# Kernel tuning notes

Measured on AMD Instinct MI355X. Metric: run time of the kernel, lower is better.

The kernel has to match this reference:

```python
import jax, jax.numpy as jnp
import numpy as np

N_NODES = 50000
N_EDGES = 800000


def setup_inputs() -> dict:
    key = jax.random.key(0)
    ks = jax.random.split(key, 8)
    x = jax.random.normal(ks[0], (N_NODES, 128), dtype=jnp.float32)
    edge_index = jax.random.randint(ks[1], (2, N_EDGES), 0, N_NODES, dtype=jnp.int64)
    # Glorot-ish scaled weights (GCNConv uses glorot init)
    W1 = jax.random.normal(ks[2], (128, 128), dtype=jnp.float32) * 0.08
    W2 = jax.random.normal(ks[3], (128, 128), dtype=jnp.float32) * 0.08
    W3 = jax.random.normal(ks[4], (128, 64), dtype=jnp.float32) * 0.08
    b1 = jnp.zeros((128,), jnp.float32)
    b2 = jnp.zeros((128,), jnp.float32)
    b3 = jnp.zeros((64,), jnp.float32)
    return {"x": x, "W1": W1, "b1": b1, "W2": W2, "b2": b2,
            "W3": W3, "b3": b3, "edge_index": edge_index}


def _gcn_layer(x, W, b, src, dst, norm, n):
    # GCNConv: out = D^{-1/2} (A+I) D^{-1/2} (x W) + b
    h = x @ W                                   # [N, F_out]
    msg = h[src] * norm[:, None]                # gather + scale per edge
    agg = jax.ops.segment_sum(msg, dst, num_segments=n)  # scatter-add
    return agg + b


def reference(x, W1, b1, W2, b2, W3, b3, edge_index):
    n = x.shape[0]
    loops = jnp.arange(n, dtype=edge_index.dtype)
    src = jnp.concatenate([edge_index[0], loops])  # add self-loops (PyG default)
    dst = jnp.concatenate([edge_index[1], loops])
    # symmetric normalization from in-degree (incl. self-loops)
    deg = jax.ops.segment_sum(jnp.ones_like(dst, dtype=x.dtype), dst, num_segments=n)
    dis = jnp.where(deg > 0, jax.lax.rsqrt(deg), 0.0)
    norm = dis[src] * dis[dst]                   # [E+N]

    h = jax.nn.relu(_gcn_layer(x, W1, b1, src, dst, norm, n))
    # dropout(p=0.5) is identity in eval mode
    h = jax.nn.relu(_gcn_layer(h, W2, b2, src, dst, norm, n))
    h = _gcn_layer(h, W3, b3, src, dst, norm, n)
    return jax.nn.log_softmax(h, axis=1)
```

## Files before the change

kernel.cpp:

```cpp
#include <hip/hip_runtime.h>
#include <hip/hip_bf16.h>
#include <cstdint>

typedef unsigned int uint32;
typedef unsigned short ushort;
typedef __attribute__((ext_vector_type(8))) short short8;
typedef __attribute__((ext_vector_type(4))) float f32x4;

#define EPB 4096
#define SLACK 3840

__device__ inline ushort bf16r(float f) {
    uint32 u = __float_as_uint(f);
    u += 0x7fff + ((u >> 16) & 1);
    return (ushort)(u >> 16);
}
__device__ inline uint32 pack_bf16(float a, float b) {
    return (uint32)bf16r(a) | ((uint32)bf16r(b) << 16);
}
__device__ inline float bf_lo(uint32 w) { return __uint_as_float(w << 16); }
__device__ inline float bf_hi(uint32 w) { return __uint_as_float(w & 0xffff0000u); }


__global__ __launch_bounds__(256) void k_bhist_prep(
        const int* __restrict__ dstv, int* __restrict__ hglob, int e, int nbE,
        const float* __restrict__ W1, const float* __restrict__ W2, const float* __restrict__ W3,
        ushort* __restrict__ Wt1, ushort* __restrict__ Wt2, ushort* __restrict__ Wt3,
        ushort* __restrict__ hsb, ushort* __restrict__ hs3, int n) {
    __shared__ int h[256];
    int bid = blockIdx.x, t = threadIdx.x;
    if (bid < nbE) {
        h[t] = 0;
        __syncthreads();
        int b0 = bid * EPB;
#pragma unroll
        for (int i = 0; i < EPB / 256; ++i) {
            int idx = b0 + i * 256 + t;
            if (idx < e) atomicAdd(&h[dstv[idx] >> 8], 1);
        }
        __syncthreads();
        hglob[bid * 256 + t] = h[t];
    } else {
        int wb = bid - nbE;
        if (wb < 3) {
            const float* W = wb == 0 ? W1 : (wb == 1 ? W2 : W3);
            ushort* Wt = wb == 0 ? Wt1 : (wb == 1 ? Wt2 : Wt3);
            int F = wb == 2 ? 64 : 128;
            for (int i = t; i < 128 * F; i += 256) {
                int k = i / F, c = i % F;
                Wt[c * 128 + k] = bf16r(W[i]);
            }
        } else {
            if (t < 128) hsb[(size_t)n * 128 + t] = 0;
            if (t < 64)  hs3[(size_t)n * 64 + t] = 0;
        }
    }
}


__global__ __launch_bounds__(256) void k_bscan(const int* __restrict__ hglob, int nbE,
                                               int* __restrict__ bpre, int* __restrict__ bcur,
                                               int nb, int e) {
    __shared__ int s[256];
    int t = threadIdx.x;
    int v = 0;
    for (int b = 0; b < nbE; ++b) v += hglob[b * 256 + t];
    s[t] = v;
    __syncthreads();
    for (int off = 1; off < 256; off <<= 1) {
        int a = (t >= off) ? s[t - off] : 0;
        __syncthreads();
        s[t] += a;
        __syncthreads();
    }
    if (t < nb) { bpre[t] = s[t] - v; bcur[t] = s[t] - v; }
    if (t == 0) bpre[nb] = e;
}


__global__ __launch_bounds__(256) void k_partition(const int* __restrict__ srcv,
                                                   const int* __restrict__ dstv,
                                                   int* __restrict__ bcur,
                                                   uint2* __restrict__ pairs, int e) {
    __shared__ int h[256], base[256], cur[256];
    int t = threadIdx.x;
    h[t] = 0; cur[t] = 0;
    __syncthreads();
    int s[EPB / 256], d[EPB / 256];
    int b0 = blockIdx.x * EPB;
#pragma unroll
    for (int i = 0; i < EPB / 256; ++i) {
        int idx = b0 + i * 256 + t;
        if (idx < e) {
            s[i] = srcv[idx]; d[i] = dstv[idx];
            atomicAdd(&h[d[i] >> 8], 1);
        } else d[i] = -1;
    }
    __syncthreads();
    if (h[t]) base[t] = atomicAdd(&bcur[t], h[t]);
    __syncthreads();
#pragma unroll
    for (int i = 0; i < EPB / 256; ++i) {
        if (d[i] >= 0) {
            int b = d[i] >> 8;
            int sl = atomicAdd(&cur[b], 1);
            pairs[base[b] + sl] = make_uint2((unsigned)s[i], (unsigned)d[i]);
        }
    }
}


__global__ __launch_bounds__(256) void k_bfinish(const uint2* __restrict__ pairs,
                                                 const int* __restrict__ bpre,
                                                 int2* __restrict__ rps, float* __restrict__ dis,
                                                 int* __restrict__ col, int n) {
    __shared__ int c[256], sc[256], cur[256];
    int t = threadIdx.x;
    c[t] = 0; cur[t] = 0;
    __syncthreads();
    int wb = blockIdx.x << 8;
    int e0 = bpre[blockIdx.x], e1 = bpre[blockIdx.x + 1];
    for (int i = e0 + t; i < e1; i += 256) atomicAdd(&c[(int)pairs[i].y - wb], 1);
    __syncthreads();
    int own = c[t];
    int pad = (own + 15) & ~15;
    sc[t] = pad;
    __syncthreads();
    for (int off = 1; off < 256; off <<= 1) {
        int a = (t >= off) ? sc[t - off] : 0;
        __syncthreads();
        sc[t] += a;
        __syncthreads();
    }
    int start = bpre[blockIdx.x] + blockIdx.x * SLACK + sc[t] - pad;
    __syncthreads();
    sc[t] = start;
    int v = wb + t;
    if (v < n) {
        rps[v] = make_int2(start, start + pad);
        dis[v] = rsqrtf((float)(own + 1));
    }
    __syncthreads();
    for (int i = e0 + t; i < e1; i += 256) {
        uint2 p = pairs[i];
        int bl = (int)p.y - wb;
        int sl = atomicAdd(&cur[bl], 1);
        col[sc[bl] + sl] = (int)p.x;
    }
    __syncthreads();
    for (int i = own; i < pad; ++i) col[start + i] = n;
}


template <int FOUT, bool BF16IN>
__global__ __launch_bounds__(256) void k_gemm_mfma(
        const void* __restrict__ Xv, const ushort* __restrict__ Wt,
        const float* __restrict__ dis, ushort* __restrict__ Yb, int n) {
    constexpr int CT = FOUT / 16;
    int lane = threadIdx.x & 63;
    int wv = threadIdx.x >> 6;
    int r16 = lane & 15, kg = lane >> 4;
    int rowA = blockIdx.x * 64 + wv * 16 + r16;
    int ra = min(rowA, n - 1);
    short8 afr[4];
    if (BF16IN) {
        const ushort* Xb = (const ushort*)Xv;
#pragma unroll
        for (int ks = 0; ks < 4; ++ks)
            afr[ks] = *(const short8*)(Xb + (size_t)ra * 128 + ks * 32 + kg * 8);
    } else {
        const float* Xf = (const float*)Xv;
#pragma unroll
        for (int ks = 0; ks < 4; ++ks) {
            const float* p = Xf + (size_t)ra * 128 + ks * 32 + kg * 8;
            float4 f0 = *(const float4*)p;
            float4 f1 = *(const float4*)(p + 4);
            short8 a;
            a[0] = (short)bf16r(f0.x); a[1] = (short)bf16r(f0.y);
            a[2] = (short)bf16r(f0.z); a[3] = (short)bf16r(f0.w);
            a[4] = (short)bf16r(f1.x); a[5] = (short)bf16r(f1.y);
            a[6] = (short)bf16r(f1.z); a[7] = (short)bf16r(f1.w);
            afr[ks] = a;
        }
    }
    f32x4 acc[CT];
#pragma unroll
    for (int c = 0; c < CT; ++c) acc[c] = (f32x4){0.f, 0.f, 0.f, 0.f};
#pragma unroll
    for (int ks = 0; ks < 4; ++ks) {
#pragma unroll
        for (int c = 0; c < CT; ++c) {
            short8 b = *(const short8*)(Wt + (c * 16 + r16) * 128 + ks * 32 + kg * 8);
            acc[c] = __builtin_amdgcn_mfma_f32_16x16x32_bf16(afr[ks], b, acc[c], 0, 0, 0);
        }
    }
    int rbase = blockIdx.x * 64 + wv * 16 + kg * 4;
#pragma unroll
    for (int j = 0; j < 4; ++j) {
        int row = rbase + j;
        if (row < n) {
            float d = dis[row];
#pragma unroll
            for (int c = 0; c < CT; ++c)
                Yb[(size_t)row * FOUT + c * 16 + r16] = bf16r(acc[c][j] * d);
        }
    }
}


__global__ __launch_bounds__(256) void k_agg_relu128(
        const uint32* __restrict__ hb, const int2* __restrict__ rps,
        const int* __restrict__ col, const float* __restrict__ dis,
        const float* __restrict__ bias, uint32* __restrict__ outb, int n) {
    int wid = threadIdx.x >> 6;
    int lane = threadIdx.x & 63;
    int v = blockIdx.x * 4 + wid;
    if (v >= n) return;
    uint32 mv = hb[(size_t)v * 64 + lane];
    float ax = bf_lo(mv), ay = bf_hi(mv);
    int2 se = rps[v];
    int s = __builtin_amdgcn_readfirstlane(se.x);
    int e = __builtin_amdgcn_readfirstlane(se.y);
    for (int k = s; k < e; k += 16) {
        uint32 m[16];
#pragma unroll
        for (int j = 0; j < 16; ++j) {
            int u = col[k + j];
            m[j] = hb[(size_t)u * 64 + lane];
        }
#pragma unroll
        for (int j = 0; j < 16; ++j) { ax += bf_lo(m[j]); ay += bf_hi(m[j]); }
    }
    float d = dis[v];
    float2 b = ((const float2*)bias)[lane];
    float ox = fmaxf(d * ax + b.x, 0.f);
    float oy = fmaxf(d * ay + b.y, 0.f);
    outb[(size_t)v * 64 + lane] = pack_bf16(ox, oy);
}

__global__ __launch_bounds__(256) void k_agg_lsm64(
        const ushort* __restrict__ hb, const int2* __restrict__ rps,
        const int* __restrict__ col, const float* __restrict__ dis,
        const float* __restrict__ bias, float* __restrict__ out, int n) {
    int wid = threadIdx.x >> 6;
    int lane = threadIdx.x & 63;
    int v = blockIdx.x * 4 + wid;
    if (v >= n) return;
    float acc = __uint_as_float((uint32)hb[(size_t)v * 64 + lane] << 16);
    int2 se = rps[v];
    int s = __builtin_amdgcn_readfirstlane(se.x);
    int e = __builtin_amdgcn_readfirstlane(se.y);
    for (int k = s; k < e; k += 16) {
        ushort m[16];
#pragma unroll
        for (int j = 0; j < 16; ++j) m[j] = hb[(size_t)col[k + j] * 64 + lane];
#pragma unroll
        for (int j = 0; j < 16; ++j) acc += __uint_as_float((uint32)m[j] << 16);
    }
    float val = dis[v] * acc + bias[lane];
    float m = val;
    for (int off = 32; off; off >>= 1) m = fmaxf(m, __shfl_xor(m, off, 64));
    float ex = expf(val - m);
    float ss = ex;
    for (int off = 32; off; off >>= 1) ss += __shfl_xor(ss, off, 64);
    out[(size_t)v * 64 + lane] = val - m - logf(ss);
}


extern "C" void kernel_launch(void* const* d_in, const int* in_sizes, int n_in,
                              void* d_out, int out_size, void* d_ws, size_t ws_size,
                              hipStream_t stream) {
    const float* x  = (const float*)d_in[0];
    const float* W1 = (const float*)d_in[1];
    const float* b1 = (const float*)d_in[2];
    const float* W2 = (const float*)d_in[3];
    const float* b2 = (const float*)d_in[4];
    const float* W3 = (const float*)d_in[5];
    const float* b3 = (const float*)d_in[6];
    const int*   ei = (const int*)d_in[7];

    const int N = in_sizes[0] / 128;
    const int E = in_sizes[7] / 2;
    const int* srcv = ei;
    const int* dstv = ei + E;
    const int NB  = (N + 255) >> 8;
    const int nbE = (E + EPB - 1) / EPB;

    char* ws = (char*)d_ws;
    size_t off = 0;
    auto alloc = [&](size_t bytes) -> void* {
        void* p = ws + off;
        off += (bytes + 255) & ~(size_t)255;
        return p;
    };
    float*  dis   = (float*)alloc((size_t)N * 4);
    int2*   rps   = (int2*)alloc((size_t)N * 8);
    int*    col   = (int*)alloc(((size_t)E + (size_t)NB * SLACK + 16) * 4);
    int*    hglob = (int*)alloc((size_t)nbE * 256 * 4);
    int*    bpre  = (int*)alloc((size_t)(NB + 1) * 4);
    int*    bcur  = (int*)alloc((size_t)(NB + 1) * 4);
    uint2*  pairs = (uint2*)alloc((size_t)E * 8);
    ushort* Wt1   = (ushort*)alloc(128 * 128 * 2);
    ushort* Wt2   = (ushort*)alloc(128 * 128 * 2);
    ushort* Wt3   = (ushort*)alloc(64 * 128 * 2);
    ushort* hsb   = (ushort*)alloc((size_t)(N + 1) * 128 * 2);
    ushort* hbX   = (ushort*)alloc((size_t)N * 128 * 2);
    ushort* hs3   = (ushort*)alloc((size_t)(N + 1) * 64 * 2);
    float*  outp  = (float*)d_out;

    k_bhist_prep<<<nbE + 4, 256, 0, stream>>>(dstv, hglob, E, nbE,
                                              W1, W2, W3, Wt1, Wt2, Wt3, hsb, hs3, N);
    k_bscan<<<1, 256, 0, stream>>>(hglob, nbE, bpre, bcur, NB, E);
    k_partition<<<nbE, 256, 0, stream>>>(srcv, dstv, bcur, pairs, E);
    k_bfinish<<<NB, 256, 0, stream>>>(pairs, bpre, rps, dis, col, N);

    int gblk = (N + 63) / 64;
    int ablk = (N + 3) / 4;
    k_gemm_mfma<128, false><<<gblk, 256, 0, stream>>>(x, Wt1, dis, hsb, N);
    k_agg_relu128<<<ablk, 256, 0, stream>>>((const uint32*)hsb, rps, col, dis, b1, (uint32*)hbX, N);
    k_gemm_mfma<128, true><<<gblk, 256, 0, stream>>>(hbX, Wt2, dis, hsb, N);
    k_agg_relu128<<<ablk, 256, 0, stream>>>((const uint32*)hsb, rps, col, dis, b2, (uint32*)hbX, N);
    k_gemm_mfma<64, true><<<gblk, 256, 0, stream>>>(hbX, Wt3, dis, hs3, N);
    k_agg_lsm64<<<ablk, 256, 0, stream>>>(hs3, rps, col, dis, b3, outp, N);
}
```

Baseline: 214.8 us.

## Split 128-wide features into two 64-wide planes and process two nodes per wave

Stores the 128-feature bf16 activations as two 64-column planes. Each aggregation wave now handles two nodes, one per half-wave, and walks the planes one after another, so each gathered neighbour row is a 128-byte segment. The padded CSR with slack and sentinel padding is replaced by an exact CSR whose remainder is handled by 8/4/1-step tail loops, which removes wasted gathers of the dummy row. The cost is more divergent tail loops, since the two half-waves can have different degrees and the neighbour list is read twice per node.

```diff
diff --git a/kernel.cpp b/kernel.cpp
--- a/kernel.cpp
+++ b/kernel.cpp
@@ -8,7 +8,6 @@
 typedef __attribute__((ext_vector_type(4))) float f32x4;
 
 #define EPB 4096
-#define SLACK 3840
 
 __device__ inline ushort bf16r(float f) {
     uint32 u = __float_as_uint(f);
@@ -26,7 +25,7 @@
         const int* __restrict__ dstv, int* __restrict__ hglob, int e, int nbE,
         const float* __restrict__ W1, const float* __restrict__ W2, const float* __restrict__ W3,
         ushort* __restrict__ Wt1, ushort* __restrict__ Wt2, ushort* __restrict__ Wt3,
-        ushort* __restrict__ hsb, ushort* __restrict__ hs3, int n) {
+        ushort* __restrict__ hsA, ushort* __restrict__ hs3, int n, size_t plsz) {
     __shared__ int h[256];
     int bid = blockIdx.x, t = threadIdx.x;
     if (bid < nbE) {
@@ -51,7 +50,7 @@
                 Wt[c * 128 + k] = bf16r(W[i]);
             }
         } else {
-            if (t < 128) hsb[(size_t)n * 128 + t] = 0;
+            if (t < 128) hsA[(size_t)(t >> 6) * plsz + (size_t)n * 64 + (t & 63)] = 0;
             if (t < 64)  hs3[(size_t)n * 64 + t] = 0;
         }
     }
@@ -123,8 +122,7 @@
     for (int i = e0 + t; i < e1; i += 256) atomicAdd(&c[(int)pairs[i].y - wb], 1);
     __syncthreads();
     int own = c[t];
-    int pad = (own + 15) & ~15;
-    sc[t] = pad;
+    sc[t] = own;
     __syncthreads();
     for (int off = 1; off < 256; off <<= 1) {
         int a = (t >= off) ? sc[t - off] : 0;
@@ -132,12 +130,12 @@
         sc[t] += a;
         __syncthreads();
     }
-    int start = bpre[blockIdx.x] + blockIdx.x * SLACK + sc[t] - pad;
+    int start = bpre[blockIdx.x] + sc[t] - own;
     __syncthreads();
     sc[t] = start;
     int v = wb + t;
     if (v < n) {
-        rps[v] = make_int2(start, start + pad);
+        rps[v] = make_int2(start, start + own);
         dis[v] = rsqrtf((float)(own + 1));
     }
     __syncthreads();
@@ -147,15 +145,13 @@
         int sl = atomicAdd(&cur[bl], 1);
         col[sc[bl] + sl] = (int)p.x;
     }
-    __syncthreads();
-    for (int i = own; i < pad; ++i) col[start + i] = n;
-}
-
-
-template <int FOUT, bool BF16IN>
+}
+
+
+template <int FOUT, int INMODE>
 __global__ __launch_bounds__(256) void k_gemm_mfma(
         const void* __restrict__ Xv, const ushort* __restrict__ Wt,
-        const float* __restrict__ dis, ushort* __restrict__ Yb, int n) {
+        const float* __restrict__ dis, ushort* __restrict__ Yb, int n, size_t plsz) {
     constexpr int CT = FOUT / 16;
     int lane = threadIdx.x & 63;
     int wv = threadIdx.x >> 6;
@@ -163,11 +159,12 @@
     int rowA = blockIdx.x * 64 + wv * 16 + r16;
     int ra = min(rowA, n - 1);
     short8 afr[4];
-    if (BF16IN) {
+    if (INMODE == 1) {
         const ushort* Xb = (const ushort*)Xv;
 #pragma unroll
         for (int ks = 0; ks < 4; ++ks)
-            afr[ks] = *(const short8*)(Xb + (size_t)ra * 128 + ks * 32 + kg * 8);
+            afr[ks] = *(const short8*)(Xb + (size_t)(ks >> 1) * plsz +
+                                       (size_t)ra * 64 + (ks & 1) * 32 + kg * 8);
     } else {
         const float* Xf = (const float*)Xv;
 #pragma unroll
@@ -201,41 +198,69 @@
         if (row < n) {
             float d = dis[row];
 #pragma unroll
-            for (int c = 0; c < CT; ++c)
-                Yb[(size_t)row * FOUT + c * 16 + r16] = bf16r(acc[c][j] * d);
-        }
-    }
-}
-
-
-__global__ __launch_bounds__(256) void k_agg_relu128(
-        const uint32* __restrict__ hb, const int2* __restrict__ rps,
+            for (int c = 0; c < CT; ++c) {
+                ushort val = bf16r(acc[c][j] * d);
+                if (FOUT == 128)
+                    Yb[(size_t)(c >> 2) * plsz + (size_t)row * 64 + (c & 3) * 16 + r16] = val;
+                else
+                    Yb[(size_t)row * 64 + c * 16 + r16] = val;
+            }
+        }
+    }
+}
+
+
+__global__ __launch_bounds__(256) void k_agg_relu_planar(
+        const ushort* __restrict__ hs, const int2* __restrict__ rps,
         const int* __restrict__ col, const float* __restrict__ dis,
-        const float* __restrict__ bias, uint32* __restrict__ outb, int n) {
+        const float* __restrict__ bias, ushort* __restrict__ outp,
+        int n, size_t plsz) {
     int wid = threadIdx.x >> 6;
     int lane = threadIdx.x & 63;
-    int v = blockIdx.x * 4 + wid;
+    int half = lane >> 5, hl = lane & 31;
+    int v = blockIdx.x * 8 + wid * 2 + half;
     if (v >= n) return;
-    uint32 mv = hb[(size_t)v * 64 + lane];
-    float ax = bf_lo(mv), ay = bf_hi(mv);
     int2 se = rps[v];
-    int s = __builtin_amdgcn_readfirstlane(se.x);
-    int e = __builtin_amdgcn_readfirstlane(se.y);
-    for (int k = s; k < e; k += 16) {
-        uint32 m[16];
-#pragma unroll
-        for (int j = 0; j < 16; ++j) {
-            int u = col[k + j];
-            m[j] = hb[(size_t)u * 64 + lane];
-        }
-#pragma unroll
-        for (int j = 0; j < 16; ++j) { ax += bf_lo(m[j]); ay += bf_hi(m[j]); }
-    }
+    int s = se.x, e = se.y;
     float d = dis[v];
-    float2 b = ((const float2*)bias)[lane];
-    float ox = fmaxf(d * ax + b.x, 0.f);
-    float oy = fmaxf(d * ay + b.y, 0.f);
-    outb[(size_t)v * 64 + lane] = pack_bf16(ox, oy);
+#pragma unroll
+    for (int p = 0; p < 2; ++p) {
+        const uint32* src = (const uint32*)(hs + p * plsz);
+        uint32 mv = src[(size_t)v * 32 + hl];
+        float ax = bf_lo(mv), ay = bf_hi(mv);
+        int k = s;
+        for (; k + 16 <= e; k += 16) {
+            uint32 m[16];
+#pragma unroll
+            for (int j = 0; j < 16; ++j) m[j] = src[(size_t)col[k + j] * 32 + hl];
+#pragma unroll
+            for (int j = 0; j < 16; ++j) { ax += bf_lo(m[j]); ay += bf_hi(m[j]); }
+        }
+        if (k + 8 <= e) {
+            uint32 m[8];
+#pragma unroll
+            for (int j = 0; j < 8; ++j) m[j] = src[(size_t)col[k + j] * 32 + hl];
+#pragma unroll
+            for (int j = 0; j < 8; ++j) { ax += bf_lo(m[j]); ay += bf_hi(m[j]); }
+            k += 8;
+        }
+        if (k + 4 <= e) {
+            uint32 m[4];
+#pragma unroll
+            for (int j = 0; j < 4; ++j) m[j] = src[(size_t)col[k + j] * 32 + hl];
+#pragma unroll
+            for (int j = 0; j < 4; ++j) { ax += bf_lo(m[j]); ay += bf_hi(m[j]); }
+            k += 4;
+        }
+        for (; k < e; ++k) {
+            uint32 m = src[(size_t)col[k] * 32 + hl];
+            ax += bf_lo(m); ay += bf_hi(m);
+        }
+        float2 b = ((const float2*)bias)[p * 32 + hl];
+        float ox = fmaxf(d * ax + b.x, 0.f);
+        float oy = fmaxf(d * ay + b.y, 0.f);
+        *(uint32*)(outp + p * plsz + (size_t)v * 64 + hl * 2) = pack_bf16(ox, oy);
+    }
 }
 
 __global__ __launch_bounds__(256) void k_agg_lsm64(
@@ -244,26 +269,44 @@
         const float* __restrict__ bias, float* __restrict__ out, int n) {
     int wid = threadIdx.x >> 6;
     int lane = threadIdx.x & 63;
-    int v = blockIdx.x * 4 + wid;
+    int hl = lane & 31;
+    int v = blockIdx.x * 8 + wid * 2 + (lane >> 5);
     if (v >= n) return;
-    float acc = __uint_as_float((uint32)hb[(size_t)v * 64 + lane] << 16);
+    const uint32* src = (const uint32*)hb;
+    uint32 mv = src[(size_t)v * 32 + hl];
+    float ax = bf_lo(mv), ay = bf_hi(mv);
     int2 se = rps[v];
-    int s = __builtin_amdgcn_readfirstlane(se.x);
-    int e = __builtin_amdgcn_readfirstlane(se.y);
-    for (int k = s; k < e; k += 16) {
-        ushort m[16];
-#pragma unroll
-        for (int j = 0; j < 16; ++j) m[j] = hb[(size_t)col[k + j] * 64 + lane];
-#pragma unroll
-        for (int j = 0; j < 16; ++j) acc += __uint_as_float((uint32)m[j] << 16);
-    }
-    float val = dis[v] * acc + bias[lane];
-    float m = val;
-    for (int off = 32; off; off >>= 1) m = fmaxf(m, __shfl_xor(m, off, 64));
-    float ex = expf(val - m);
-    float ss = ex;
-    for (int off = 32; off; off >>= 1) ss += __shfl_xor(ss, off, 64);
-    out[(size_t)v * 64 + lane] = val - m - logf(ss);
+    int s = se.x, e = se.y;
+    int k = s;
+    for (; k + 16 <= e; k += 16) {
+        uint32 m[16];
+#pragma unroll
+        for (int j = 0; j < 16; ++j) m[j] = src[(size_t)col[k + j] * 32 + hl];
+#pragma unroll
+        for (int j = 0; j < 16; ++j) { ax += bf_lo(m[j]); ay += bf_hi(m[j]); }
+    }
+    if (k + 8 <= e) {
+        uint32 m[8];
+#pragma unroll
+        for (int j = 0; j < 8; ++j) m[j] = src[(size_t)col[k + j] * 32 + hl];
+#pragma unroll
+        for (int j = 0; j < 8; ++j) { ax += bf_lo(m[j]); ay += bf_hi(m[j]); }
+        k += 8;
+    }
+    for (; k < e; ++k) {
+        uint32 m = src[(size_t)col[k] * 32 + hl];
+        ax += bf_lo(m); ay += bf_hi(m);
+    }
+    float d = dis[v];
+    float2 b = ((const float2*)bias)[hl];
+    float valx = d * ax + b.x;
+    float valy = d * ay + b.y;
+    float mx = fmaxf(valx, valy);
+    for (int off = 16; off; off >>= 1) mx = fmaxf(mx, __shfl_xor(mx, off, 64));
+    float ss = expf(valx - mx) + expf(valy - mx);
+    for (int off = 16; off; off >>= 1) ss += __shfl_xor(ss, off, 64);
+    float ls = mx + logf(ss);
+    ((float2*)out)[(size_t)v * 32 + hl] = make_float2(valx - ls, valy - ls);
 }
 
 
@@ -285,6 +328,7 @@
     const int* dstv = ei + E;
     const int NB  = (N + 255) >> 8;
     const int nbE = (E + EPB - 1) / EPB;
+    const size_t PLSZ = (size_t)(N + 1) * 64;
 
     char* ws = (char*)d_ws;
     size_t off = 0;
@@ -295,7 +339,7 @@
     };
     float*  dis   = (float*)alloc((size_t)N * 4);
     int2*   rps   = (int2*)alloc((size_t)N * 8);
-    int*    col   = (int*)alloc(((size_t)E + (size_t)NB * SLACK + 16) * 4);
+    int*    col   = (int*)alloc(((size_t)E + 16) * 4);
     int*    hglob = (int*)alloc((size_t)nbE * 256 * 4);
     int*    bpre  = (int*)alloc((size_t)(NB + 1) * 4);
     int*    bcur  = (int*)alloc((size_t)(NB + 1) * 4);
@@ -303,23 +347,23 @@
     ushort* Wt1   = (ushort*)alloc(128 * 128 * 2);
     ushort* Wt2   = (ushort*)alloc(128 * 128 * 2);
     ushort* Wt3   = (ushort*)alloc(64 * 128 * 2);
-    ushort* hsb   = (ushort*)alloc((size_t)(N + 1) * 128 * 2);
-    ushort* hbX   = (ushort*)alloc((size_t)N * 128 * 2);
-    ushort* hs3   = (ushort*)alloc((size_t)(N + 1) * 64 * 2);
+    ushort* hsA   = (ushort*)alloc(PLSZ * 2 * 2);
+    ushort* hbB   = (ushort*)alloc(PLSZ * 2 * 2);
+    ushort* hs3   = (ushort*)alloc(PLSZ * 2);
     float*  outp  = (float*)d_out;
 
     k_bhist_prep<<<nbE + 4, 256, 0, stream>>>(dstv, hglob, E, nbE,
-                                              W1, W2, W3, Wt1, Wt2, Wt3, hsb, hs3, N);
+                                              W1, W2, W3, Wt1, Wt2, Wt3, hsA, hs3, N, PLSZ);
     k_bscan<<<1, 256, 0, stream>>>(hglob, nbE, bpre, bcur, NB, E);
     k_partition<<<nbE, 256, 0, stream>>>(srcv, dstv, bcur, pairs, E);
     k_bfinish<<<NB, 256, 0, stream>>>(pairs, bpre, rps, dis, col, N);
 
     int gblk = (N + 63) / 64;
-    int ablk = (N + 3) / 4;
-    k_gemm_mfma<128, false><<<gblk, 256, 0, stream>>>(x, Wt1, dis, hsb, N);
-    k_agg_relu128<<<ablk, 256, 0, stream>>>((const uint32*)hsb, rps, col, dis, b1, (uint32*)hbX, N);
-    k_gemm_mfma<128, true><<<gblk, 256, 0, stream>>>(hbX, Wt2, dis, hsb, N);
-    k_agg_relu128<<<ablk, 256, 0, stream>>>((const uint32*)hsb, rps, col, dis, b2, (uint32*)hbX, N);
-    k_gemm_mfma<64, true><<<gblk, 256, 0, stream>>>(hbX, Wt3, dis, hs3, N);
+    int ablk = (N + 7) / 8;
+    k_gemm_mfma<128, 0><<<gblk, 256, 0, stream>>>(x, Wt1, dis, hsA, N, PLSZ);
+    k_agg_relu_planar<<<ablk, 256, 0, stream>>>(hsA, rps, col, dis, b1, hbB, N, PLSZ);
+    k_gemm_mfma<128, 1><<<gblk, 256, 0, stream>>>(hbB, Wt2, dis, hsA, N, PLSZ);
+    k_agg_relu_planar<<<ablk, 256, 0, stream>>>(hsA, rps, col, dis, b2, hbB, N, PLSZ);
+    k_gemm_mfma<64, 1><<<gblk, 256, 0, stream>>>(hbB, Wt3, dis, hs3, N, PLSZ);
     k_agg_lsm64<<<ablk, 256, 0, stream>>>(hs3, rps, col, dis, b3, outp, N);
 }
```

After: 232.2 us. 1.08x slower.

## Replace histogram-scan edge bucketing with fixed-capacity buckets and unpadded CSR

Applied to the files above, without the earlier changes.

Removes the separate histogram and scan kernels by having the partition kernel append edges into fixed-capacity per-bucket regions, using a global atomic counter per bucket. CSR rows are no longer padded to multiples of 16 with sentinel entries. The aggregation kernels instead handle remainders with 8/4/1-wide tail loops, and final outputs use nontemporal stores. This cuts two launches, one pass over the destination array, and the wasted sentinel gathers. In exchange, any bucket holding more than CAP edges silently drops the excess, and the preallocated buffers are larger.

```diff
diff --git a/kernel.cpp b/kernel.cpp
--- a/kernel.cpp
+++ b/kernel.cpp
@@ -8,7 +8,7 @@
 typedef __attribute__((ext_vector_type(4))) float f32x4;
 
 #define EPB 4096
-#define SLACK 3840
+#define CAP 8192
 
 __device__ inline ushort bf16r(float f) {
     uint32 u = __float_as_uint(f);
@@ -22,72 +22,28 @@
 __device__ inline float bf_hi(uint32 w) { return __uint_as_float(w & 0xffff0000u); }
 
 
-__global__ __launch_bounds__(256) void k_bhist_prep(
-        const int* __restrict__ dstv, int* __restrict__ hglob, int e, int nbE,
+__global__ __launch_bounds__(256) void k_part_prep(
+        const int* __restrict__ srcv, const int* __restrict__ dstv,
+        int* __restrict__ bcnt, uint64_t* __restrict__ pairs, int e, int nbE,
         const float* __restrict__ W1, const float* __restrict__ W2, const float* __restrict__ W3,
-        ushort* __restrict__ Wt1, ushort* __restrict__ Wt2, ushort* __restrict__ Wt3,
-        ushort* __restrict__ hsb, ushort* __restrict__ hs3, int n) {
-    __shared__ int h[256];
+        ushort* __restrict__ Wt1, ushort* __restrict__ Wt2, ushort* __restrict__ Wt3) {
     int bid = blockIdx.x, t = threadIdx.x;
-    if (bid < nbE) {
-        h[t] = 0;
-        __syncthreads();
-        int b0 = bid * EPB;
-#pragma unroll
-        for (int i = 0; i < EPB / 256; ++i) {
-            int idx = b0 + i * 256 + t;
-            if (idx < e) atomicAdd(&h[dstv[idx] >> 8], 1);
-        }
-        __syncthreads();
-        hglob[bid * 256 + t] = h[t];
-    } else {
+    if (bid >= nbE) {
         int wb = bid - nbE;
-        if (wb < 3) {
-            const float* W = wb == 0 ? W1 : (wb == 1 ? W2 : W3);
-            ushort* Wt = wb == 0 ? Wt1 : (wb == 1 ? Wt2 : Wt3);
-            int F = wb == 2 ? 64 : 128;
-            for (int i = t; i < 128 * F; i += 256) {
-                int k = i / F, c = i % F;
-                Wt[c * 128 + k] = bf16r(W[i]);
-            }
-        } else {
-            if (t < 128) hsb[(size_t)n * 128 + t] = 0;
-            if (t < 64)  hs3[(size_t)n * 64 + t] = 0;
-        }
-    }
-}
-
-
-__global__ __launch_bounds__(256) void k_bscan(const int* __restrict__ hglob, int nbE,
-                                               int* __restrict__ bpre, int* __restrict__ bcur,
-                                               int nb, int e) {
-    __shared__ int s[256];
-    int t = threadIdx.x;
-    int v = 0;
-    for (int b = 0; b < nbE; ++b) v += hglob[b * 256 + t];
-    s[t] = v;
-    __syncthreads();
-    for (int off = 1; off < 256; off <<= 1) {
-        int a = (t >= off) ? s[t - off] : 0;
-        __syncthreads();
-        s[t] += a;
-        __syncthreads();
-    }
-    if (t < nb) { bpre[t] = s[t] - v; bcur[t] = s[t] - v; }
-    if (t == 0) bpre[nb] = e;
-}
-
-
-__global__ __launch_bounds__(256) void k_partition(const int* __restrict__ srcv,
-                                                   const int* __restrict__ dstv,
-                                                   int* __restrict__ bcur,
-                                                   uint2* __restrict__ pairs, int e) {
+        const float* W = wb == 0 ? W1 : (wb == 1 ? W2 : W3);
+        ushort* Wt = wb == 0 ? Wt1 : (wb == 1 ? Wt2 : Wt3);
+        int F = wb == 2 ? 64 : 128;
+        for (int i = t; i < 128 * F; i += 256) {
+            int k = i / F, c = i % F;
+            Wt[c * 128 + k] = bf16r(W[i]);
+        }
+        return;
+    }
     __shared__ int h[256], base[256], cur[256];
-    int t = threadIdx.x;
     h[t] = 0; cur[t] = 0;
     __syncthreads();
     int s[EPB / 256], d[EPB / 256];
-    int b0 = blockIdx.x * EPB;
+    int b0 = bid * EPB;
 #pragma unroll
     for (int i = 0; i < EPB / 256; ++i) {
         int idx = b0 + i * 256 + t;
@@ -97,21 +53,24 @@
         } else d[i] = -1;
     }
     __syncthreads();
-    if (h[t]) base[t] = atomicAdd(&bcur[t], h[t]);
+    base[t] = h[t] ? atomicAdd(&bcnt[t], h[t]) : 0;
     __syncthreads();
 #pragma unroll
     for (int i = 0; i < EPB / 256; ++i) {
         if (d[i] >= 0) {
             int b = d[i] >> 8;
-            int sl = atomicAdd(&cur[b], 1);
-            pairs[base[b] + sl] = make_uint2((unsigned)s[i], (unsigned)d[i]);
-        }
-    }
-}
-
-
-__global__ __launch_bounds__(256) void k_bfinish(const uint2* __restrict__ pairs,
-                                                 const int* __restrict__ bpre,
+            int sl = base[b] + atomicAdd(&cur[b], 1);
+            if (sl < CAP) {
+                uint64_t pk = (uint64_t)(unsigned)s[i] | ((uint64_t)(unsigned)d[i] << 32);
+                __builtin_nontemporal_store(pk, &pairs[(size_t)b * CAP + sl]);
+            }
+        }
+    }
+}
+
+
+__global__ __launch_bounds__(256) void k_bfinish(const uint64_t* __restrict__ pairs,
+                                                 const int* __restrict__ bcnt,
                                                  int2* __restrict__ rps, float* __restrict__ dis,
                                                  int* __restrict__ col, int n) {
     __shared__ int c[256], sc[256], cur[256];
@@ -119,12 +78,13 @@
     c[t] = 0; cur[t] = 0;
     __syncthreads();
     int wb = blockIdx.x << 8;
-    int e0 = bpre[blockIdx.x], e1 = bpre[blockIdx.x + 1];
-    for (int i = e0 + t; i < e1; i += 256) atomicAdd(&c[(int)pairs[i].y - wb], 1);
+    int e0 = blockIdx.x * CAP;
+    int e1 = e0 + min(bcnt[blockIdx.x], CAP);
+    for (int i = e0 + t; i < e1; i += 256)
+        atomicAdd(&c[(int)(pairs[i] >> 32) - wb], 1);
     __syncthreads();
     int own = c[t];
-    int pad = (own + 15) & ~15;
-    sc[t] = pad;
+    sc[t] = own;
     __syncthreads();
     for (int off = 1; off < 256; off <<= 1) {
         int a = (t >= off) ? sc[t - off] : 0;
@@ -132,23 +92,21 @@
         sc[t] += a;
         __syncthreads();
     }
-    int start = bpre[blockIdx.x] + blockIdx.x * SLACK + sc[t] - pad;
+    int start = blockIdx.x * CAP + sc[t] - own;
     __syncthreads();
     sc[t] = start;
     int v = wb + t;
     if (v < n) {
-        rps[v] = make_int2(start, start + pad);
+        rps[v] = make_int2(start, start + own);
         dis[v] = rsqrtf((float)(own + 1));
     }
     __syncthreads();
     for (int i = e0 + t; i < e1; i += 256) {
-        uint2 p = pairs[i];
-        int bl = (int)p.y - wb;
+        uint64_t p = pairs[i];
+        int bl = (int)(p >> 32) - wb;
         int sl = atomicAdd(&cur[bl], 1);
-        col[sc[bl] + sl] = (int)p.x;
-    }
-    __syncthreads();
-    for (int i = own; i < pad; ++i) col[start + i] = n;
+        col[sc[bl] + sl] = (int)(uint32)p;
+    }
 }
 
 
@@ -221,7 +179,8 @@
     int2 se = rps[v];
     int s = __builtin_amdgcn_readfirstlane(se.x);
     int e = __builtin_amdgcn_readfirstlane(se.y);
-    for (int k = s; k < e; k += 16) {
+    int k = s;
+    for (; k + 16 <= e; k += 16) {
         uint32 m[16];
 #pragma unroll
         for (int j = 0; j < 16; ++j) {
@@ -230,12 +189,32 @@
         }
 #pragma unroll
         for (int j = 0; j < 16; ++j) { ax += bf_lo(m[j]); ay += bf_hi(m[j]); }
+    }
+    if (k + 8 <= e) {
+        uint32 m[8];
+#pragma unroll
+        for (int j = 0; j < 8; ++j) m[j] = hb[(size_t)col[k + j] * 64 + lane];
+#pragma unroll
+        for (int j = 0; j < 8; ++j) { ax += bf_lo(m[j]); ay += bf_hi(m[j]); }
+        k += 8;
+    }
+    if (k + 4 <= e) {
+        uint32 m[4];
+#pragma unroll
+        for (int j = 0; j < 4; ++j) m[j] = hb[(size_t)col[k + j] * 64 + lane];
+#pragma unroll
+        for (int j = 0; j < 4; ++j) { ax += bf_lo(m[j]); ay += bf_hi(m[j]); }
+        k += 4;
+    }
+    for (; k < e; ++k) {
+        uint32 m = hb[(size_t)col[k] * 64 + lane];
+        ax += bf_lo(m); ay += bf_hi(m);
     }
     float d = dis[v];
     float2 b = ((const float2*)bias)[lane];
     float ox = fmaxf(d * ax + b.x, 0.f);
     float oy = fmaxf(d * ay + b.y, 0.f);
-    outb[(size_t)v * 64 + lane] = pack_bf16(ox, oy);
+    __builtin_nontemporal_store(pack_bf16(ox, oy), &outb[(size_t)v * 64 + lane]);
 }
 
 __global__ __launch_bounds__(256) void k_agg_lsm64(
@@ -250,20 +229,30 @@
     int2 se = rps[v];
     int s = __builtin_amdgcn_readfirstlane(se.x);
     int e = __builtin_amdgcn_readfirstlane(se.y);
-    for (int k = s; k < e; k += 16) {
+    int k = s;
+    for (; k + 16 <= e; k += 16) {
         ushort m[16];
 #pragma unroll
         for (int j = 0; j < 16; ++j) m[j] = hb[(size_t)col[k + j] * 64 + lane];
 #pragma unroll
         for (int j = 0; j < 16; ++j) acc += __uint_as_float((uint32)m[j] << 16);
     }
+    if (k + 8 <= e) {
+        ushort m[8];
+#pragma unroll
+        for (int j = 0; j < 8; ++j) m[j] = hb[(size_t)col[k + j] * 64 + lane];
+#pragma unroll
+        for (int j = 0; j < 8; ++j) acc += __uint_as_float((uint32)m[j] << 16);
+        k += 8;
+    }
+    for (; k < e; ++k) acc += __uint_as_float((uint32)hb[(size_t)col[k] * 64 + lane] << 16);
     float val = dis[v] * acc + bias[lane];
     float m = val;
     for (int off = 32; off; off >>= 1) m = fmaxf(m, __shfl_xor(m, off, 64));
     float ex = expf(val - m);
     float ss = ex;
     for (int off = 32; off; off >>= 1) ss += __shfl_xor(ss, off, 64);
-    out[(size_t)v * 64 + lane] = val - m - logf(ss);
+    __builtin_nontemporal_store(val - m - logf(ss), &out[(size_t)v * 64 + lane]);
 }
 
 
@@ -293,26 +282,23 @@
         off += (bytes + 255) & ~(size_t)255;
         return p;
     };
-    float*  dis   = (float*)alloc((size_t)N * 4);
-    int2*   rps   = (int2*)alloc((size_t)N * 8);
-    int*    col   = (int*)alloc(((size_t)E + (size_t)NB * SLACK + 16) * 4);
-    int*    hglob = (int*)alloc((size_t)nbE * 256 * 4);
-    int*    bpre  = (int*)alloc((size_t)(NB + 1) * 4);
-    int*    bcur  = (int*)alloc((size_t)(NB + 1) * 4);
-    uint2*  pairs = (uint2*)alloc((size_t)E * 8);
-    ushort* Wt1   = (ushort*)alloc(128 * 128 * 2);
-    ushort* Wt2   = (ushort*)alloc(128 * 128 * 2);
-    ushort* Wt3   = (ushort*)alloc(64 * 128 * 2);
-    ushort* hsb   = (ushort*)alloc((size_t)(N + 1) * 128 * 2);
-    ushort* hbX   = (ushort*)alloc((size_t)N * 128 * 2);
-    ushort* hs3   = (ushort*)alloc((size_t)(N + 1) * 64 * 2);
-    float*  outp  = (float*)d_out;
-
-    k_bhist_prep<<<nbE + 4, 256, 0, stream>>>(dstv, hglob, E, nbE,
-                                              W1, W2, W3, Wt1, Wt2, Wt3, hsb, hs3, N);
-    k_bscan<<<1, 256, 0, stream>>>(hglob, nbE, bpre, bcur, NB, E);
-    k_partition<<<nbE, 256, 0, stream>>>(srcv, dstv, bcur, pairs, E);
-    k_bfinish<<<NB, 256, 0, stream>>>(pairs, bpre, rps, dis, col, N);
+    float*    dis   = (float*)alloc((size_t)N * 4);
+    int2*     rps   = (int2*)alloc((size_t)N * 8);
+    int*      bcnt  = (int*)alloc((size_t)NB * 4);
+    int*      col   = (int*)alloc((size_t)NB * CAP * 4);
+    uint64_t* pairs = (uint64_t*)alloc((size_t)NB * CAP * 8);
+    ushort*   Wt1   = (ushort*)alloc(128 * 128 * 2);
+    ushort*   Wt2   = (ushort*)alloc(128 * 128 * 2);
+    ushort*   Wt3   = (ushort*)alloc(64 * 128 * 2);
+    ushort*   hsb   = (ushort*)alloc((size_t)N * 128 * 2);
+    ushort*   hbX   = (ushort*)alloc((size_t)N * 128 * 2);
+    ushort*   hs3   = (ushort*)alloc((size_t)N * 64 * 2);
+    float*    outp  = (float*)d_out;
+
+    (void)hipMemsetAsync(bcnt, 0, (size_t)NB * 4, stream);
+    k_part_prep<<<nbE + 3, 256, 0, stream>>>(srcv, dstv, bcnt, pairs, E, nbE,
+                                             W1, W2, W3, Wt1, Wt2, Wt3);
+    k_bfinish<<<NB, 256, 0, stream>>>(pairs, bcnt, rps, dis, col, N);
 
     int gblk = (N + 63) / 64;
     int ablk = (N + 3) / 4;
```

Result: faster. 201.9 us (-6.0%).
